# Kernel tuning notes

Measured on AMD Instinct MI355X. Metric: run time of the kernel, lower is better.

Reference implementation:

```python
import jax, jax.numpy as jnp
import numpy as np
import math

B, LS, G, KNN, DIM, PE, H, DH = 2, 2048, 32, 16, 256, 32, 8, 32
INNER = H * DH
FF = 4 * DIM
EPS = 1e-5


def _ln(x, g, b):
    m = jnp.mean(x, -1, keepdims=True)
    v = jnp.var(x, -1, keepdims=True)
    return (x - m) / jnp.sqrt(v + EPS) * g + b


def _ff(x, w1, b1, w2, b2):
    return jax.nn.gelu(x @ w1 + b1) @ w2 + b2


def setup_inputs():
    key = jax.random.key(0)
    ks = jax.random.split(key, 20)
    def w(i, shape):
        return jax.random.normal(ks[i], shape, jnp.float32) * 0.02
    return {
        'latents': jax.random.normal(ks[0], (B, LS + G, DIM), jnp.float32),
        'topk_indices': jax.random.randint(ks[1], (B, LS, KNN), 0, LS),
        'rpe': jax.random.normal(ks[2], (B, LS, KNN, PE), jnp.float32),
        'self_rpe': jax.random.normal(ks[3], (B, LS, 1, PE), jnp.float32),
        'distances': jax.random.uniform(ks[4], (B, LS, KNN), jnp.float32) * 10.0,
        'num_spatial': LS,
        'sa_wq': w(5, (DIM, INNER)), 'sa_wk': w(6, (DIM + PE, INNER)),
        'sa_wv': w(7, (DIM + PE, INNER)), 'sa_wo': w(8, (INNER, DIM)),
        'sa_bo': jnp.zeros((DIM,)),
        'sa_log_sigma': jnp.full((H,), math.log(3.0), jnp.float32),
        'sa_gbias': jnp.asarray(0.0, jnp.float32),
        'ln1_g': jnp.ones((DIM,)), 'ln1_b': jnp.zeros((DIM,)),
        'ln2_g': jnp.ones((DIM,)), 'ln2_b': jnp.zeros((DIM,)),
        'sff_w1': w(9, (DIM, FF)), 'sff_b1': jnp.zeros((FF,)),
        'sff_w2': w(10, (FF, DIM)), 'sff_b2': jnp.zeros((DIM,)),
        'ga_wq': w(11, (DIM, INNER)), 'ga_wk': w(12, (DIM, INNER)),
        'ga_wv': w(13, (DIM, INNER)), 'ga_wo': w(14, (INNER, DIM)),
        'ga_bo': jnp.zeros((DIM,)),
        'ga_gbias': jnp.asarray(0.0, jnp.float32),
        'ln3_g': jnp.ones((DIM,)), 'ln3_b': jnp.zeros((DIM,)),
        'ln4_g': jnp.ones((DIM,)), 'ln4_b': jnp.zeros((DIM,)),
        'gff_w1': w(15, (DIM, FF)), 'gff_b1': jnp.zeros((FF,)),
        'gff_w2': w(16, (FF, DIM)), 'gff_b2': jnp.zeros((DIM,)),
    }


def _forward(latents, topk_indices, rpe, self_rpe, distances, num_spatial, p):
    L = num_spatial
    spatial = latents[:, :L]
    glob = latents[:, L:]
    b, _, d = spatial.shape
    g = glob.shape[1]
    scale = DH ** -0.5
    # ---- spatial local attention: context = [self, kNN neighbors, all globals] ----
    x = _ln(spatial, p['ln1_g'], p['ln1_b'])
    neighbors = jax.vmap(lambda s, idx: s[idx])(x, topk_indices)  # [B,L,k,D] gather
    glob_exp = jnp.broadcast_to(glob[:, None], (b, L, g, d))
    ctx = jnp.concatenate([x[:, :, None, :], neighbors, glob_exp], axis=2)  # [B,L,1+k+G,D]
    rpe_cat = jnp.concatenate([self_rpe, rpe, jnp.zeros((b, L, g, PE), x.dtype)], axis=2)
    ctx = jnp.concatenate([ctx, rpe_cat], axis=-1)  # [B,L,C,D+PE]
    q = (x @ p['sa_wq']).reshape(b, L, H, DH)
    kk = (ctx @ p['sa_wk']).reshape(b, L, -1, H, DH)
    vv = (ctx @ p['sa_wv']).reshape(b, L, -1, H, DH)
    attn = jnp.einsum('blhd,blchd->bhlc', q, kk) * scale
    sigma_sq = jnp.exp(2.0 * p['sa_log_sigma'])  # [H]
    dist_sp = jnp.concatenate([jnp.zeros((b, L, 1), x.dtype), distances], axis=2)  # [B,L,1+k]
    gauss = -(dist_sp ** 2)[:, None] / (2.0 * sigma_sq[None, :, None, None])  # [B,H,L,1+k]
    bias = jnp.concatenate([gauss, jnp.broadcast_to(p['sa_gbias'], (b, H, L, g))], axis=-1)
    attn = jax.nn.softmax(attn + bias, axis=-1)
    out = jnp.einsum('bhlc,blchd->blhd', attn, vv).reshape(b, L, INNER)
    spatial = spatial + out @ p['sa_wo'] + p['sa_bo']
    spatial = spatial + _ff(_ln(spatial, p['ln2_g'], p['ln2_b']), p['sff_w1'], p['sff_b1'], p['sff_w2'], p['sff_b2'])
    # ---- global full attention: Q=global, K/V=[updated spatial; normed global] ----
    gq_in = _ln(glob, p['ln3_g'], p['ln3_b'])
    kv = jnp.concatenate([spatial, gq_in], axis=1)  # [B,L+G,D]
    qg = (gq_in @ p['ga_wq']).reshape(b, g, H, DH)
    kg = (kv @ p['ga_wk']).reshape(b, L + g, H, DH)
    vg = (kv @ p['ga_wv']).reshape(b, L + g, H, DH)
    a2 = jnp.einsum('bghd,bchd->bhgc', qg, kg) * scale + p['ga_gbias']
    a2 = jax.nn.softmax(a2, axis=-1)
    og = jnp.einsum('bhgc,bchd->bghd', a2, vg).reshape(b, g, INNER)
    glob = glob + og @ p['ga_wo'] + p['ga_bo']
    glob = glob + _ff(_ln(glob, p['ln4_g'], p['ln4_b']), p['gff_w1'], p['gff_b1'], p['gff_w2'], p['gff_b2'])
    return jnp.concatenate([spatial, glob], axis=1)


def reference(latents, topk_indices, rpe, self_rpe, distances, num_spatial,
              sa_wq, sa_wk, sa_wv, sa_wo, sa_bo, sa_log_sigma, sa_gbias,
              ln1_g, ln1_b, ln2_g, ln2_b, sff_w1, sff_b1, sff_w2, sff_b2,
              ga_wq, ga_wk, ga_wv, ga_wo, ga_bo, ga_gbias,
              ln3_g, ln3_b, ln4_g, ln4_b, gff_w1, gff_b1, gff_w2, gff_b2):
    p = dict(sa_wq=sa_wq, sa_wk=sa_wk, sa_wv=sa_wv, sa_wo=sa_wo, sa_bo=sa_bo,
             sa_log_sigma=sa_log_sigma, sa_gbias=sa_gbias,
             ln1_g=ln1_g, ln1_b=ln1_b, ln2_g=ln2_g, ln2_b=ln2_b,
             sff_w1=sff_w1, sff_b1=sff_b1, sff_w2=sff_w2, sff_b2=sff_b2,
             ga_wq=ga_wq, ga_wk=ga_wk, ga_wv=ga_wv, ga_wo=ga_wo, ga_bo=ga_bo,
             ga_gbias=ga_gbias, ln3_g=ln3_g, ln3_b=ln3_b, ln4_g=ln4_g, ln4_b=ln4_b,
             gff_w1=gff_w1, gff_b1=gff_b1, gff_w2=gff_w2, gff_b2=gff_b2)
    return _forward(latents, topk_indices, rpe, self_rpe, distances, num_spatial, p)
```

## Files before the change

kernel.cpp:

```cpp
#include <hip/hip_runtime.h>
#include <math.h>

#define LS 2048
#define NG 32
#define ROWS_B 2080
#define DIM 256
#define PE 32
#define NH 8
#define DH 32
#define NCTX 49
#define SCALE 0.17677669529663687f

typedef __attribute__((ext_vector_type(8))) short short8;
typedef __attribute__((ext_vector_type(4))) float f32x4;
typedef __attribute__((ext_vector_type(4))) unsigned short us4;

__device__ __forceinline__ unsigned short f2bf(float x)
{
    unsigned int u = __float_as_uint(x);
    unsigned int r = (u + 0x7fffu + ((u >> 16) & 1u)) >> 16;
    return (unsigned short)r;
}
__device__ __forceinline__ float bf2f(unsigned short v)
{
    return __uint_as_float((unsigned int)v << 16);
}
__device__ __forceinline__ float4 bf2f4(us4 v)
{
    return (float4){ bf2f(v.x), bf2f(v.y), bf2f(v.z), bf2f(v.w) };
}
__device__ __forceinline__ float dot4(float4 a, float4 b)
{
    return a.x * b.x + a.y * b.y + a.z * b.z + a.w * b.w;
}
__device__ __forceinline__ float gelu_f(float x)
{
    float x3 = x * x * x;
    return 0.5f * x * (1.0f + tanhf(0.7978845608028654f * (x + 0.044715f * x3)));
}

struct WEnt { const float* src; unsigned short* dst; int K; int N; int t0; };
struct WTab { WEnt e[9]; };

__global__ __launch_bounds__(256) void wprep_k(
    WTab tab,
    const float* __restrict__ sa_wq, const float* __restrict__ sa_wk,
    const float* __restrict__ sa_wv, const float* __restrict__ sa_wo,
    unsigned short* __restrict__ wt_qkvw, unsigned short* __restrict__ wt_wo2,
    const float* __restrict__ latents,
    const float* __restrict__ g1, const float* __restrict__ b1,
    const float* __restrict__ g3, const float* __restrict__ b3,
    float* __restrict__ X, float* __restrict__ GQ)
{
    __shared__ unsigned short tile[64][72];
    __shared__ float red[8];
    int blk = blockIdx.x, t = threadIdx.x;
    if (blk < 512) {
        const float* wkpe = sa_wk + 256 * 256;
        const float* wvpe = sa_wv + 256 * 256;
        if (blk < 256) {
            int j = blk, h = j >> 5, p = j & 31;
            const float* wq = sa_wq + (size_t)t * 256 + h * 32;
            const float* wk = wkpe + (size_t)p * 256 + h * 32;
            float acc = 0.0f;
            #pragma unroll
            for (int dd = 0; dd < 32; ++dd) acc += wq[dd] * wk[dd];
            wt_qkvw[(size_t)(768 + j) * 256 + t] = f2bf(acc);
        } else {
            int n = blk - 256;
            #pragma unroll
            for (int kk = 0; kk < 2; ++kk) {
                int k = t + kk * 256;
                float v;
                if (k < 256) v = sa_wo[(size_t)k * 256 + n];
                else {
                    int j = k - 256, h = j >> 5, p = j & 31;
                    float a = 0.0f;
                    #pragma unroll
                    for (int dd = 0; dd < 32; ++dd)
                        a += wvpe[(size_t)p * 256 + h * 32 + dd] * sa_wo[(size_t)(h * 32 + dd) * 256 + n];
                    v = a;
                }
                wt_wo2[(size_t)n * 512 + k] = f2bf(v);
            }
        }
    } else if (blk < 736) {
        int local0 = blk - 512;
        int i = 0;
        #pragma unroll
        for (int j = 1; j < 9; ++j) if (local0 >= tab.e[j].t0) i = j;
        const float* W = tab.e[i].src;
        unsigned short* Wt = tab.e[i].dst;
        int K = tab.e[i].K, N = tab.e[i].N;
        int local = local0 - tab.e[i].t0;
        int nb = N >> 6;
        int n0 = (local % nb) * 64, k0 = (local / nb) * 64;
        #pragma unroll
        for (int r = 0; r < 4; ++r) {
            int k = r * 16 + (t >> 4);
            int n = (t & 15) * 4;
            float4 wv = *(const float4*)(W + (size_t)(k0 + k) * N + n0 + n);
            tile[k][n + 0] = f2bf(wv.x);
            tile[k][n + 1] = f2bf(wv.y);
            tile[k][n + 2] = f2bf(wv.z);
            tile[k][n + 3] = f2bf(wv.w);
        }
        __syncthreads();
        #pragma unroll
        for (int r = 0; r < 4; ++r) {
            int n = r * 16 + (t >> 4);
            int k = (t & 15) * 4;
            us4 o;
            o.x = tile[k + 0][n];
            o.y = tile[k + 1][n];
            o.z = tile[k + 2][n];
            o.w = tile[k + 3][n];
            *(us4*)(Wt + (size_t)(n0 + n) * K + k0 + k) = o;
        }
    } else {
        int blk2 = blk - 736;
        const float* gam; const float* bet; size_t ip; float* op;
        if (blk2 < 4096) {
            int b = blk2 >> 11;
            ip = ((size_t)b * ROWS_B + (blk2 & 2047)) * DIM + t;
            op = X + (size_t)blk2 * DIM + t;
            gam = g1; bet = b1;
        } else {
            int r2 = blk2 - 4096;
            int b = r2 >> 5;
            ip = ((size_t)b * ROWS_B + LS + (r2 & 31)) * DIM + t;
            op = GQ + (size_t)r2 * DIM + t;
            gam = g3; bet = b3;
        }
        float v = latents[ip];
        float a = v, b2 = v * v;
        #pragma unroll
        for (int m = 32; m >= 1; m >>= 1) { a += __shfl_xor(a, m); b2 += __shfl_xor(b2, m); }
        if ((t & 63) == 0) { red[t >> 6] = a; red[4 + (t >> 6)] = b2; }
        __syncthreads();
        float mean = (red[0] + red[1] + red[2] + red[3]) * (1.0f / 256.0f);
        float var  = (red[4] + red[5] + red[6] + red[7]) * (1.0f / 256.0f) - mean * mean;
        *op = (v - mean) * rsqrtf(var + 1e-5f) * gam[t] + bet[t];
    }
}

__global__ __launch_bounds__(256) void ln_rows_k(
    const float* __restrict__ in, const float* __restrict__ gam,
    const float* __restrict__ bet, float* __restrict__ out)
{
    __shared__ float red[8];
    int r = blockIdx.x, t = threadIdx.x;
    int b = r >> 11;
    size_t ip = ((size_t)b * ROWS_B + (r & 2047)) * DIM + t;
    float v = in[ip];
    float a = v, b2 = v * v;
    #pragma unroll
    for (int m = 32; m >= 1; m >>= 1) { a += __shfl_xor(a, m); b2 += __shfl_xor(b2, m); }
    if ((t & 63) == 0) { red[t >> 6] = a; red[4 + (t >> 6)] = b2; }
    __syncthreads();
    float mean = (red[0] + red[1] + red[2] + red[3]) * (1.0f / 256.0f);
    float var  = (red[4] + red[5] + red[6] + red[7]) * (1.0f / 256.0f) - mean * mean;
    out[(size_t)r * DIM + t] = (v - mean) * rsqrtf(var + 1e-5f) * gam[t] + bet[t];
}

__global__ __launch_bounds__(256) void wgs_k(
    const unsigned short* __restrict__ wtq, const unsigned short* __restrict__ kvglb,
    unsigned short* __restrict__ wgs)
{
    int n = blockIdx.x, k = threadIdx.x;
    int h = n & 7, cg = n >> 3;
    float acc = 0.0f;
    #pragma unroll
    for (int dd = 0; dd < 32; ++dd)
        acc += bf2f(wtq[(size_t)(h * 32 + dd) * 256 + k]) * bf2f(kvglb[(size_t)cg * 512 + h * 32 + dd]);
    wgs[(size_t)n * 256 + k] = f2bf(acc);
}

template<int BIAS, int DOGELU, int RES, int ABF16, int CBF16>
__global__ __launch_bounds__(256) void mgemm_k(
    const void* __restrict__ Av, const unsigned short* __restrict__ Bt,
    const float* __restrict__ bias, const float* __restrict__ Res,
    void* __restrict__ Cv, int M, int N, int K, int bstr,
    int arpb, int absr, int aoff, int crpb, int cbsr, int coff)
{
    __shared__ unsigned short Asl[64][64];
    __shared__ unsigned short Bsl[64][64];
    int t = threadIdx.x;
    int col0 = blockIdx.x * 64, row0 = blockIdx.y * 64;
    int lane = t & 63, w = t >> 6;
    int wr = w >> 1, wc = w & 1;
    int lrow = lane & 15, lk = lane >> 4;

    int srow = t >> 4;
    int scol = (t & 15) << 2;
    int sslot = (t & 15) >> 1;
    int shalf = (t & 15) & 1;

    f32x4 acc[2][2];
    #pragma unroll
    for (int m = 0; m < 2; ++m)
        #pragma unroll
        for (int n = 0; n < 2; ++n)
            acc[m][n] = (f32x4){0.f, 0.f, 0.f, 0.f};

    for (int kk = 0; kk < K; kk += 64) {
        #pragma unroll
        for (int r = 0; r < 4; ++r) {
            int row = r * 16 + srow;
            int ar = row0 + row;
            size_t ab = ((size_t)(ar / arpb) * absr + aoff + (ar % arpb)) * (size_t)K + kk + scol;
            us4 ap;
            if (ABF16) {
                ap = *(const us4*)((const unsigned short*)Av + ab);
            } else {
                float4 av = *(const float4*)((const float*)Av + ab);
                ap.x = f2bf(av.x); ap.y = f2bf(av.y); ap.z = f2bf(av.z); ap.w = f2bf(av.w);
            }
            *(us4*)&Asl[row][((sslot ^ (row & 7)) << 3) + (shalf << 2)] = ap;
            us4 bv = *(const us4*)(Bt + (size_t)(col0 + row) * bstr + kk + scol);
            *(us4*)&Bsl[row][((sslot ^ (row & 7)) << 3) + (shalf << 2)] = bv;
        }
        __syncthreads();
        #pragma unroll
        for (int k2 = 0; k2 < 2; ++k2) {
            short8 af[2], bfr[2];
            #pragma unroll
            for (int m = 0; m < 2; ++m) {
                int rowA = wr * 32 + m * 16 + lrow;
                af[m] = *(short8*)&Asl[rowA][((k2 * 4 + lk) ^ (rowA & 7)) << 3];
                int rowB = wc * 32 + m * 16 + lrow;
                bfr[m] = *(short8*)&Bsl[rowB][((k2 * 4 + lk) ^ (rowB & 7)) << 3];
            }
            #pragma unroll
            for (int m = 0; m < 2; ++m)
                #pragma unroll
                for (int n = 0; n < 2; ++n)
                    acc[m][n] = __builtin_amdgcn_mfma_f32_16x16x32_bf16(af[m], bfr[n], acc[m][n], 0, 0, 0);
        }
        __syncthreads();
    }
    #pragma unroll
    for (int m = 0; m < 2; ++m) {
        #pragma unroll
        for (int n = 0; n < 2; ++n) {
            int col = col0 + wc * 32 + n * 16 + lrow;
            #pragma unroll
            for (int j = 0; j < 4; ++j) {
                int r = row0 + wr * 32 + m * 16 + lk * 4 + j;
                size_t cp = ((size_t)(r / crpb) * cbsr + coff + (r % crpb)) * (size_t)N + col;
                float o = acc[m][n][j];
                if (BIAS)   o += bias[col];
                if (DOGELU) o = gelu_f(o);
                if (RES)    o += Res[cp];
                if (CBF16) ((unsigned short*)Cv)[cp] = f2bf(o);
                else       ((float*)Cv)[cp] = o;
            }
        }
    }
}

__global__ __launch_bounds__(256) void attn_sp_k(
    const unsigned short* __restrict__ QKV, const unsigned short* __restrict__ KVGLb,
    const unsigned short* __restrict__ GSb, const int* __restrict__ idx,
    const float* __restrict__ rpe, const float* __restrict__ srpe,
    const float* __restrict__ dist, const float* __restrict__ lsig,
    const float* __restrict__ gbias, unsigned short* __restrict__ ORb)
{
    __shared__ float s_rpe[17 * 32];
    __shared__ float s_sc[NCTX * 8];
    __shared__ float s_red[32 * 64];
    __shared__ float s_d[16];
    __shared__ int   s_row[17];
    int t = threadIdx.x;
    int r = blockIdx.x;
    int b = r >> 11;
    int w = t >> 6, lane = t & 63;
    int h = lane >> 3, dg = lane & 7;

    if (t < 32) s_rpe[t] = srpe[(size_t)r * 32 + t];
    for (int i = t; i < 512; i += 256) s_rpe[32 + i] = rpe[(size_t)r * 512 + i];
    if (t < 16) {
        s_row[t + 1] = (b << 11) + idx[r * 16 + t];
        s_d[t] = dist[(size_t)r * 16 + t];
    }
    if (t == 16) s_row[0] = r;

    size_t qb = (size_t)r * 1024 + lane * 4;
    float4 q4  = bf2f4(*(const us4*)(QKV + qb));
    float4 qw4 = bf2f4(*(const us4*)(QKV + qb + 768));
    float inv2s = 1.0f / (2.0f * __expf(2.0f * lsig[h]));
    float gb = gbias[0];
    __syncthreads();

    us4 kreg[5];
    #pragma unroll
    for (int i = 0; i < 5; ++i) {
        int c = w + 4 * i;
        if (c < 17) kreg[i] = *(const us4*)(QKV + (size_t)s_row[c] * 1024 + 256 + lane * 4);
    }
    float sc_loc[5];
    #pragma unroll
    for (int i = 0; i < 5; ++i) {
        int c = w + 4 * i;
        if (c < 17) {
            float4 k4 = bf2f4(kreg[i]);
            float4 rv4 = *(const float4*)&s_rpe[c * 32 + dg * 4];
            float part = dot4(q4, k4) + dot4(rv4, qw4);
            part += __shfl_xor(part, 1);
            part += __shfl_xor(part, 2);
            part += __shfl_xor(part, 4);
            float bia = (c == 0) ? 0.0f : -s_d[c - 1] * s_d[c - 1] * inv2s;
            float sval = part * SCALE + bia;
            if (dg == 0) s_sc[c * 8 + h] = sval;
            sc_loc[i] = sval;
        }
    }
    float sc_glob[8];
    #pragma unroll
    for (int i = 0; i < 8; ++i) {
        int gi = w + 4 * i;
        float sval = bf2f(GSb[(size_t)r * 512 + (((size_t)b * 32 + gi) << 3) + h]) * SCALE + gb;
        if (dg == 0) s_sc[(17 + gi) * 8 + h] = sval;
        sc_glob[i] = sval;
    }
    __syncthreads();

    float vals[7];
    float lm = -3.0e38f;
    #pragma unroll
    for (int i = 0; i < 7; ++i) {
        int cc = dg + 8 * i;
        if (cc < NCTX) { float v = s_sc[cc * 8 + h]; vals[i] = v; lm = fmaxf(lm, v); }
    }
    lm = fmaxf(lm, __shfl_xor(lm, 1));
    lm = fmaxf(lm, __shfl_xor(lm, 2));
    lm = fmaxf(lm, __shfl_xor(lm, 4));
    float ls = 0.0f;
    #pragma unroll
    for (int i = 0; i < 7; ++i) {
        int cc = dg + 8 * i;
        if (cc < NCTX) ls += __expf(vals[i] - lm);
    }
    ls += __shfl_xor(ls, 1);
    ls += __shfl_xor(ls, 2);
    ls += __shfl_xor(ls, 4);
    float inv = 1.0f / ls;

    us4 vreg[5];
    #pragma unroll
    for (int i = 0; i < 5; ++i) {
        int c = w + 4 * i;
        if (c < 17) vreg[i] = *(const us4*)(QKV + (size_t)s_row[c] * 1024 + 512 + lane * 4);
    }
    float4 acc4 = (float4){0, 0, 0, 0}, racc4 = (float4){0, 0, 0, 0};
    #pragma unroll
    for (int i = 0; i < 5; ++i) {
        int c = w + 4 * i;
        if (c < 17) {
            float p = __expf(sc_loc[i] - lm);
            float4 v4 = bf2f4(vreg[i]);
            float4 rv4 = *(const float4*)&s_rpe[c * 32 + dg * 4];
            racc4.x += p * rv4.x; racc4.y += p * rv4.y;
            racc4.z += p * rv4.z; racc4.w += p * rv4.w;
            acc4.x += p * v4.x; acc4.y += p * v4.y;
            acc4.z += p * v4.z; acc4.w += p * v4.w;
        }
    }
    #pragma unroll
    for (int i = 0; i < 8; ++i) {
        int gi = w + 4 * i;
        float p = __expf(sc_glob[i] - lm);
        float4 v4 = bf2f4(*(const us4*)(KVGLb + ((size_t)(b * NG + gi)) * 512 + 256 + lane * 4));
        acc4.x += p * v4.x; acc4.y += p * v4.y;
        acc4.z += p * v4.z; acc4.w += p * v4.w;
    }

    s_red[(w * 8 + 0) * 64 + lane] = acc4.x;
    s_red[(w * 8 + 1) * 64 + lane] = acc4.y;
    s_red[(w * 8 + 2) * 64 + lane] = acc4.z;
    s_red[(w * 8 + 3) * 64 + lane] = acc4.w;
    s_red[(w * 8 + 4) * 64 + lane] = racc4.x;
    s_red[(w * 8 + 5) * 64 + lane] = racc4.y;
    s_red[(w * 8 + 6) * 64 + lane] = racc4.z;
    s_red[(w * 8 + 7) * 64 + lane] = racc4.w;
    __syncthreads();
    {
        int j = w;
        float a = 0.0f, rr = 0.0f;
        #pragma unroll
        for (int ww = 0; ww < 4; ++ww) {
            a  += s_red[(ww * 8 + j) * 64 + lane];
            rr += s_red[(ww * 8 + 4 + j) * 64 + lane];
        }
        int e = h * 32 + dg * 4 + j;
        ORb[(size_t)r * 512 + e]       = f2bf(a * inv);
        ORb[(size_t)r * 512 + 256 + e] = f2bf(rr * inv);
    }
}

__global__ __launch_bounds__(256) void ga_scores_k(
    const unsigned short* __restrict__ GKVQ, const unsigned short* __restrict__ KVG,
    float* __restrict__ A2)
{
    int t = threadIdx.x;
    int bh = blockIdx.x;
    int b = bh >> 3, h = bh & 7;
    int w = t >> 6, lane = t & 63;
    int ct = blockIdx.y * 4 + w;
    if (ct >= 130) return;
    int lr = lane & 15, lq = lane >> 4;

    short8 aq0 = *(const short8*)(GKVQ + ((size_t)(b * 32 + lr)) * 768 + 512 + h * 32 + lq * 8);
    short8 aq1 = *(const short8*)(GKVQ + ((size_t)(b * 32 + 16 + lr)) * 768 + 512 + h * 32 + lq * 8);
    int c = ct * 16 + lr;
    const unsigned short* kr = (c < LS)
        ? KVG + ((size_t)(b * LS + c)) * 512 + h * 32 + lq * 8
        : GKVQ + ((size_t)(b * NG + (c - LS))) * 768 + h * 32 + lq * 8;
    short8 bk = *(const short8*)kr;

    f32x4 acc0 = (f32x4){0, 0, 0, 0}, acc1 = (f32x4){0, 0, 0, 0};
    acc0 = __builtin_amdgcn_mfma_f32_16x16x32_bf16(aq0, bk, acc0, 0, 0, 0);
    acc1 = __builtin_amdgcn_mfma_f32_16x16x32_bf16(aq1, bk, acc1, 0, 0, 0);

    float* arow = A2 + ((size_t)(b * NH + h) * NG) * ROWS_B + ct * 16 + lr;
    #pragma unroll
    for (int j = 0; j < 4; ++j) {
        arow[(size_t)(lq * 4 + j) * ROWS_B]        = acc0[j] * SCALE;
        arow[(size_t)(16 + lq * 4 + j) * ROWS_B]   = acc1[j] * SCALE;
    }
}

__global__ __launch_bounds__(256) void ga_softmax_k(float* __restrict__ A2)
{
    __shared__ float red[8];
    int t = threadIdx.x;
    float* row = A2 + (size_t)blockIdx.x * ROWS_B;
    float lm = -1e30f;
    for (int i = t; i < ROWS_B; i += 256) lm = fmaxf(lm, row[i]);
    #pragma unroll
    for (int m = 32; m >= 1; m >>= 1) lm = fmaxf(lm, __shfl_xor(lm, m));
    if ((t & 63) == 0) red[t >> 6] = lm;
    __syncthreads();
    float M = fmaxf(fmaxf(red[0], red[1]), fmaxf(red[2], red[3]));
    float ls = 0.0f;
    for (int i = t; i < ROWS_B; i += 256) {
        float e = __expf(row[i] - M);
        row[i] = e;
        ls += e;
    }
    #pragma unroll
    for (int m = 32; m >= 1; m >>= 1) ls += __shfl_xor(ls, m);
    if ((t & 63) == 0) red[4 + (t >> 6)] = ls;
    __syncthreads();
    float inv = 1.0f / (red[4] + red[5] + red[6] + red[7]);
    for (int i = t; i < ROWS_B; i += 256) row[i] *= inv;
}

__global__ __launch_bounds__(256) void ga_wv_k(
    const float* __restrict__ A2, const unsigned short* __restrict__ GKVQ,
    const unsigned short* __restrict__ KVG, float* __restrict__ OGP)
{
    __shared__ float s_acc[8][256];
    int t = threadIdx.x;
    int bg = blockIdx.x;
    int s = blockIdx.y;
    int b = bg >> 5, g = bg & 31;
    int tt = t & 31, sub = t >> 5;
    int h = tt >> 2;
    const float* w = A2 + ((size_t)(b * NH + h) * NG + g) * ROWS_B;
    int c0 = s * 65, cend = c0 + 65;
    float acc[8] = {};
    for (int c = c0 + sub; c < cend; c += 8) {
        float p = w[c];
        const unsigned short* vr = (c < LS)
            ? KVG + ((size_t)(b * LS + c)) * 512 + 256 + tt * 8
            : GKVQ + ((size_t)(b * NG + (c - LS))) * 768 + 256 + tt * 8;
        us4 v0 = *(const us4*)vr;
        us4 v1 = *(const us4*)(vr + 4);
        acc[0] += p * bf2f(v0.x); acc[1] += p * bf2f(v0.y);
        acc[2] += p * bf2f(v0.z); acc[3] += p * bf2f(v0.w);
        acc[4] += p * bf2f(v1.x); acc[5] += p * bf2f(v1.y);
        acc[6] += p * bf2f(v1.z); acc[7] += p * bf2f(v1.w);
    }
    #pragma unroll
    for (int j = 0; j < 8; ++j) s_acc[sub][tt * 8 + j] = acc[j];
    __syncthreads();
    float o = 0.0f;
    #pragma unroll
    for (int ss = 0; ss < 8; ++ss) o += s_acc[ss][t];
    OGP[((size_t)bg * 32 + s) * 256 + t] = o;
}

__global__ __launch_bounds__(1024) void glob_tail_k(
    const float* __restrict__ OGP, const float* __restrict__ latents,
    const float* __restrict__ ga_wo, const float* __restrict__ ga_bo,
    const float* __restrict__ ln4g, const float* __restrict__ ln4b,
    const float* __restrict__ w1, const float* __restrict__ b1,
    const float* __restrict__ w2, const float* __restrict__ b2,
    float* __restrict__ GTP)
{
    __shared__ float s_part[4][256];
    __shared__ float s_og[256];
    __shared__ float s_y[256];
    __shared__ float s_h1[256];
    __shared__ float red[16];
    int bg = blockIdx.x, q = blockIdx.y, t = threadIdx.x;
    int tt = t & 255, grp = t >> 8;

    float og = 0.0f;
    #pragma unroll
    for (int s = 0; s < 8; ++s)
        og += OGP[((size_t)bg * 32 + grp * 8 + s) * 256 + tt];
    s_part[grp][tt] = og;
    __syncthreads();
    if (grp == 0) s_og[tt] = s_part[0][tt] + s_part[1][tt] + s_part[2][tt] + s_part[3][tt];
    __syncthreads();

    float x = 0.0f;
    {
        int k0 = grp * 64;
        #pragma unroll 16
        for (int k = k0; k < k0 + 64; ++k) x += s_og[k] * ga_wo[(size_t)k * 256 + tt];
    }
    s_part[grp][tt] = x;
    __syncthreads();
    int b = bg >> 5;
    size_t row = (size_t)b * ROWS_B + LS + (bg & 31);
    float res = latents[row * 256 + tt]
              + s_part[0][tt] + s_part[1][tt] + s_part[2][tt] + s_part[3][tt] + ga_bo[tt];

    float a = res, b2s = res * res;
    #pragma unroll
    for (int m = 32; m >= 1; m >>= 1) { a += __shfl_xor(a, m); b2s += __shfl_xor(b2s, m); }
    if ((t & 63) == 0 && t < 256) { red[t >> 6] = a; red[8 + (t >> 6)] = b2s; }
    __syncthreads();
    float mean = (red[0] + red[1] + red[2] + red[3]) * (1.0f / 256.0f);
    float var  = (red[8] + red[9] + red[10] + red[11]) * (1.0f / 256.0f) - mean * mean;
    float y = (res - mean) * rsqrtf(var + 1e-5f) * ln4g[tt] + ln4b[tt];
    if (grp == 0) s_y[tt] = y;
    __syncthreads();

    float h1p = 0.0f;
    {
        int k0 = grp * 64;
        #pragma unroll 16
        for (int k = k0; k < k0 + 64; ++k) h1p += s_y[k] * w1[(size_t)k * 1024 + q * 256 + tt];
    }
    s_part[grp][tt] = h1p;
    __syncthreads();
    if (grp == 0)
        s_h1[tt] = gelu_f(b1[q * 256 + tt]
                 + s_part[0][tt] + s_part[1][tt] + s_part[2][tt] + s_part[3][tt]);
    __syncthreads();

    float o = 0.0f;
    {
        int j0 = grp * 64;
        #pragma unroll 16
        for (int j = j0; j < j0 + 64; ++j) o += s_h1[j] * w2[(size_t)(q * 256 + j) * 256 + tt];
    }
    s_part[grp][tt] = o;
    __syncthreads();
    if (grp == 0) {
        float v = s_part[0][tt] + s_part[1][tt] + s_part[2][tt] + s_part[3][tt];
        if (q == 0) v += res + b2[tt];
        GTP[((size_t)bg * 4 + q) * 256 + tt] = v;
    }
}

__global__ __launch_bounds__(256) void glob_fin_k(
    const float* __restrict__ GTP, float* __restrict__ out)
{
    int bg = blockIdx.x, t = threadIdx.x;
    int b = bg >> 5;
    size_t row = (size_t)b * ROWS_B + LS + (bg & 31);
    float v = GTP[((size_t)bg * 4 + 0) * 256 + t] + GTP[((size_t)bg * 4 + 1) * 256 + t]
            + GTP[((size_t)bg * 4 + 2) * 256 + t] + GTP[((size_t)bg * 4 + 3) * 256 + t];
    out[row * 256 + t] = v;
}

extern "C" void kernel_launch(void* const* d_in, const int* in_sizes, int n_in,
                              void* d_out, int out_size, void* d_ws, size_t ws_size,
                              hipStream_t stream)
{
    const float* latents = (const float*)d_in[0];
    const int*   idx     = (const int*)d_in[1];
    const float* rpe     = (const float*)d_in[2];
    const float* srpe    = (const float*)d_in[3];
    const float* dist    = (const float*)d_in[4];
    const float* sa_wq   = (const float*)d_in[6];
    const float* sa_wk   = (const float*)d_in[7];
    const float* sa_wv   = (const float*)d_in[8];
    const float* sa_wo   = (const float*)d_in[9];
    const float* sa_bo   = (const float*)d_in[10];
    const float* lsig    = (const float*)d_in[11];
    const float* gbias   = (const float*)d_in[12];
    const float* ln1g    = (const float*)d_in[13];
    const float* ln1b    = (const float*)d_in[14];
    const float* ln2g    = (const float*)d_in[15];
    const float* ln2b    = (const float*)d_in[16];
    const float* sff_w1  = (const float*)d_in[17];
    const float* sff_b1  = (const float*)d_in[18];
    const float* sff_w2  = (const float*)d_in[19];
    const float* sff_b2  = (const float*)d_in[20];
    const float* ga_wq   = (const float*)d_in[21];
    const float* ga_wk   = (const float*)d_in[22];
    const float* ga_wv   = (const float*)d_in[23];
    const float* ga_wo   = (const float*)d_in[24];
    const float* ga_bo   = (const float*)d_in[25];
    const float* ln3g    = (const float*)d_in[27];
    const float* ln3b    = (const float*)d_in[28];
    const float* ln4g    = (const float*)d_in[29];
    const float* ln4b    = (const float*)d_in[30];
    const float* gff_w1  = (const float*)d_in[31];
    const float* gff_b1  = (const float*)d_in[32];
    const float* gff_w2  = (const float*)d_in[33];
    const float* gff_b2  = (const float*)d_in[34];
    float* out = (float*)d_out;

    const size_t SZ = (size_t)4096 * 256;
    float* ws = (float*)d_ws;
    float* X = ws;
    unsigned short* QKVb = (unsigned short*)(ws + SZ);
    unsigned short* H1b  = QKVb;
    unsigned short* KVGb = QKVb;
    unsigned short* ORb  = (unsigned short*)(ws + 3 * SZ);
    unsigned short* GSb  = (unsigned short*)(ws + 4 * SZ);
    float* A2  = ws + 3 * SZ;
    float* OGP = A2 + (size_t)2 * NH * NG * ROWS_B;
    float* GTP = OGP + (size_t)64 * 32 * 256;
    unsigned short* wt = (unsigned short*)(ws + 5 * SZ);
    unsigned short* wt_qkvw = wt;
    unsigned short* wt_ff1  = wt + 262144;
    unsigned short* wt_ff2  = wt + 524288;
    unsigned short* wt_gakv = wt + 786432;
    unsigned short* wt_wo2  = wt + 983040;
    unsigned short* wgs_w   = wt + 1114112;
    float* smalls = ws + 5 * SZ + 622592;
    unsigned short* KVGLb = (unsigned short*)smalls;
    float* GQ = smalls + 16384;
    unsigned short* GKVQb = (unsigned short*)(GQ + 16384);

    dim3 blk(256);

    WTab tab;
    tab.e[0] = { sa_wq,  wt_qkvw,           256,  256,   0 };
    tab.e[1] = { sa_wk,  wt_qkvw + 65536,   256,  256,  16 };
    tab.e[2] = { sa_wv,  wt_qkvw + 131072,  256,  256,  32 };
    tab.e[3] = { sff_w1, wt_ff1,            256, 1024,  48 };
    tab.e[4] = { sff_w2, wt_ff2,           1024,  256, 112 };
    tab.e[5] = { ga_wk,  wt_gakv,           256,  256, 176 };
    tab.e[6] = { ga_wv,  wt_gakv + 65536,   256,  256, 192 };
    tab.e[7] = { ga_wq,  wt_gakv + 131072,  256,  256, 208 };
    tab.e[8] = { sa_wq,  wt_qkvw,           256,  256, 1 << 30 };

    wprep_k<<<dim3(4896), blk, 0, stream>>>(tab, sa_wq, sa_wk, sa_wv, sa_wo,
                                            wt_qkvw, wt_wo2, latents,
                                            ln1g, ln1b, ln3g, ln3b, X, GQ);

    mgemm_k<0,0,0,0,1><<<dim3(8,1), blk, 0, stream>>>(latents, wt_qkvw + 65536, nullptr, nullptr, KVGLb,
        64,512,256,256, 32,ROWS_B,LS, 64,64,0);
    wgs_k<<<dim3(512), blk, 0, stream>>>(wt_qkvw, KVGLb, wgs_w);

    mgemm_k<0,0,0,0,1><<<dim3(16,64), blk, 0, stream>>>(X, wt_qkvw, nullptr, nullptr, QKVb,
        4096,1024,256,256, 4096,4096,0, 4096,4096,0);
    mgemm_k<0,0,0,0,1><<<dim3(8,64), blk, 0, stream>>>(X, wgs_w, nullptr, nullptr, GSb,
        4096,512,256,256, 4096,4096,0, 4096,4096,0);

    attn_sp_k<<<dim3(4096), blk, 0, stream>>>(QKVb, KVGLb, GSb, idx, rpe, srpe, dist,
                                              lsig, gbias, ORb);

    mgemm_k<1,0,1,1,0><<<dim3(4,64), blk, 0, stream>>>(ORb, wt_wo2, sa_bo, latents, out,
        4096,256,512,512, 4096,4096,0, LS,ROWS_B,0);

    ln_rows_k<<<dim3(4096), blk, 0, stream>>>(out, ln2g, ln2b, X);
    mgemm_k<1,1,0,0,1><<<dim3(16,64), blk, 0, stream>>>(X, wt_ff1, sff_b1, nullptr, H1b,
        4096,1024,256,256, 4096,4096,0, 4096,4096,0);
    mgemm_k<1,0,1,1,0><<<dim3(4,64), blk, 0, stream>>>(H1b, wt_ff2, sff_b2, out, out,
        4096,256,1024,1024, 4096,4096,0, LS,ROWS_B,0);

    mgemm_k<0,0,0,0,1><<<dim3(8,64), blk, 0, stream>>>(out, wt_gakv, nullptr, nullptr, KVGb,
        4096,512,256,256, LS,ROWS_B,0, 4096,4096,0);
    mgemm_k<0,0,0,0,1><<<dim3(12,1), blk, 0, stream>>>(GQ, wt_gakv, nullptr, nullptr, GKVQb,
        64,768,256,256, 64,64,0, 64,64,0);

    ga_scores_k<<<dim3(16, 33), blk, 0, stream>>>(GKVQb, KVGb, A2);
    ga_softmax_k<<<dim3(512), blk, 0, stream>>>(A2);
    ga_wv_k<<<dim3(64, 32), blk, 0, stream>>>(A2, GKVQb, KVGb, OGP);

    glob_tail_k<<<dim3(64, 4), dim3(1024), 0, stream>>>(OGP, latents, ga_wo, ga_bo, ln4g, ln4b,
                                                        gff_w1, gff_b1, gff_w2, gff_b2, GTP);
    glob_fin_k<<<dim3(64), blk, 0, stream>>>(GTP, out);
}
```

Measured before the change: 169.9 us.

## Fuse QKV and global-score GEMMs and switch large GEMMs to 128-row tiles

The global-score projection weights are placed right after the QKV weights, so a single GEMM writes a 1536-wide row holding Q, K, V, QW and the global scores. The attention kernel now reads the scores from that combined buffer at a new stride. A new 128x64-tile MFMA GEMM replaces the 64x64 version for the large projections, reusing B tiles over more rows and halving the block count. Each block carries more accumulators, which may lower occupancy, and the grids shrink to 128–768 blocks.

```diff
diff --git a/kernel.cpp b/kernel.cpp
--- a/kernel.cpp
+++ b/kernel.cpp
@@ -10,6 +10,7 @@
 #define DH 32
 #define NCTX 49
 #define SCALE 0.17677669529663687f
+#define QSTR 1536
 
 typedef __attribute__((ext_vector_type(8))) short short8;
 typedef __attribute__((ext_vector_type(4))) float f32x4;
@@ -259,12 +260,102 @@
     }
 }
 
+template<int BIAS, int DOGELU, int RES, int ABF16, int CBF16>
+__global__ __launch_bounds__(256) void mgemm128_k(
+    const void* __restrict__ Av, const unsigned short* __restrict__ Bt,
+    const float* __restrict__ bias, const float* __restrict__ Res,
+    void* __restrict__ Cv, int M, int N, int K, int bstr,
+    int arpb, int absr, int aoff, int crpb, int cbsr, int coff)
+{
+    __shared__ unsigned short Asl[128][64];
+    __shared__ unsigned short Bsl[64][64];
+    int t = threadIdx.x;
+    int col0 = blockIdx.x * 64, row0 = blockIdx.y * 128;
+    int lane = t & 63, w = t >> 6;
+    int wr = w >> 1, wc = w & 1;
+    int lrow = lane & 15, lk = lane >> 4;
+
+    int srow = t >> 4;
+    int scol = (t & 15) << 2;
+    int sslot = (t & 15) >> 1;
+    int shalf = (t & 15) & 1;
+
+    f32x4 acc[4][2];
+    #pragma unroll
+    for (int m = 0; m < 4; ++m)
+        #pragma unroll
+        for (int n = 0; n < 2; ++n)
+            acc[m][n] = (f32x4){0.f, 0.f, 0.f, 0.f};
+
+    for (int kk = 0; kk < K; kk += 64) {
+        #pragma unroll
+        for (int r = 0; r < 8; ++r) {
+            int row = r * 16 + srow;
+            int ar = row0 + row;
+            size_t ab = ((size_t)(ar / arpb) * absr + aoff + (ar % arpb)) * (size_t)K + kk + scol;
+            us4 ap;
+            if (ABF16) {
+                ap = *(const us4*)((const unsigned short*)Av + ab);
+            } else {
+                float4 av = *(const float4*)((const float*)Av + ab);
+                ap.x = f2bf(av.x); ap.y = f2bf(av.y); ap.z = f2bf(av.z); ap.w = f2bf(av.w);
+            }
+            *(us4*)&Asl[row][((sslot ^ (row & 7)) << 3) + (shalf << 2)] = ap;
+        }
+        #pragma unroll
+        for (int r = 0; r < 4; ++r) {
+            int row = r * 16 + srow;
+            us4 bv = *(const us4*)(Bt + (size_t)(col0 + row) * bstr + kk + scol);
+            *(us4*)&Bsl[row][((sslot ^ (row & 7)) << 3) + (shalf << 2)] = bv;
+        }
+        __syncthreads();
+        #pragma unroll
+        for (int k2 = 0; k2 < 2; ++k2) {
+            short8 af[4], bfr[2];
+            #pragma unroll
+            for (int m = 0; m < 4; ++m) {
+                int rowA = wr * 64 + m * 16 + lrow;
+                af[m] = *(short8*)&Asl[rowA][((k2 * 4 + lk) ^ (rowA & 7)) << 3];
+            }
+            #pragma unroll
+            for (int n = 0; n < 2; ++n) {
+                int rowB = wc * 32 + n * 16 + lrow;
+                bfr[n] = *(short8*)&Bsl[rowB][((k2 * 4 + lk) ^ (rowB & 7)) << 3];
+            }
+            #pragma unroll
+            for (int m = 0; m < 4; ++m)
+                #pragma unroll
+                for (int n = 0; n < 2; ++n)
+                    acc[m][n] = __builtin_amdgcn_mfma_f32_16x16x32_bf16(af[m], bfr[n], acc[m][n], 0, 0, 0);
+        }
+        __syncthreads();
+    }
+    #pragma unroll
+    for (int m = 0; m < 4; ++m) {
+        #pragma unroll
+        for (int n = 0; n < 2; ++n) {
+            int col = col0 + wc * 32 + n * 16 + lrow;
+            #pragma unroll
+            for (int j = 0; j < 4; ++j) {
+                int r = row0 + wr * 64 + m * 16 + lk * 4 + j;
+                size_t cp = ((size_t)(r / crpb) * cbsr + coff + (r % crpb)) * (size_t)N + col;
+                float o = acc[m][n][j];
+                if (BIAS)   o += bias[col];
+                if (DOGELU) o = gelu_f(o);
+                if (RES)    o += Res[cp];
+                if (CBF16) ((unsigned short*)Cv)[cp] = f2bf(o);
+                else       ((float*)Cv)[cp] = o;
+            }
+        }
+    }
+}
+
 __global__ __launch_bounds__(256) void attn_sp_k(
     const unsigned short* __restrict__ QKV, const unsigned short* __restrict__ KVGLb,
-    const unsigned short* __restrict__ GSb, const int* __restrict__ idx,
-    const float* __restrict__ rpe, const float* __restrict__ srpe,
-    const float* __restrict__ dist, const float* __restrict__ lsig,
-    const float* __restrict__ gbias, unsigned short* __restrict__ ORb)
+    const int* __restrict__ idx, const float* __restrict__ rpe,
+    const float* __restrict__ srpe, const float* __restrict__ dist,
+    const float* __restrict__ lsig, const float* __restrict__ gbias,
+    unsigned short* __restrict__ ORb)
 {
     __shared__ float s_rpe[17 * 32];
     __shared__ float s_sc[NCTX * 8];
@@ -285,7 +376,7 @@
     }
     if (t == 16) s_row[0] = r;
 
-    size_t qb = (size_t)r * 1024 + lane * 4;
+    size_t qb = (size_t)r * QSTR + lane * 4;
     float4 q4  = bf2f4(*(const us4*)(QKV + qb));
     float4 qw4 = bf2f4(*(const us4*)(QKV + qb + 768));
     float inv2s = 1.0f / (2.0f * __expf(2.0f * lsig[h]));
@@ -296,7 +387,7 @@
     #pragma unroll
     for (int i = 0; i < 5; ++i) {
         int c = w + 4 * i;
-        if (c < 17) kreg[i] = *(const us4*)(QKV + (size_t)s_row[c] * 1024 + 256 + lane * 4);
+        if (c < 17) kreg[i] = *(const us4*)(QKV + (size_t)s_row[c] * QSTR + 256 + lane * 4);
     }
     float sc_loc[5];
     #pragma unroll
@@ -319,7 +410,7 @@
     #pragma unroll
     for (int i = 0; i < 8; ++i) {
         int gi = w + 4 * i;
-        float sval = bf2f(GSb[(size_t)r * 512 + (((size_t)b * 32 + gi) << 3) + h]) * SCALE + gb;
+        float sval = bf2f(QKV[(size_t)r * QSTR + 1024 + (((size_t)b * 32 + gi) << 3) + h]) * SCALE + gb;
         if (dg == 0) s_sc[(17 + gi) * 8 + h] = sval;
         sc_glob[i] = sval;
     }
@@ -350,7 +441,7 @@
     #pragma unroll
     for (int i = 0; i < 5; ++i) {
         int c = w + 4 * i;
-        if (c < 17) vreg[i] = *(const us4*)(QKV + (size_t)s_row[c] * 1024 + 512 + lane * 4);
+        if (c < 17) vreg[i] = *(const us4*)(QKV + (size_t)s_row[c] * QSTR + 512 + lane * 4);
     }
     float4 acc4 = (float4){0, 0, 0, 0}, racc4 = (float4){0, 0, 0, 0};
     #pragma unroll
@@ -621,22 +712,21 @@
     const size_t SZ = (size_t)4096 * 256;
     float* ws = (float*)d_ws;
     float* X = ws;
-    unsigned short* QKVb = (unsigned short*)(ws + SZ);
-    unsigned short* H1b  = QKVb;
-    unsigned short* KVGb = QKVb;
-    unsigned short* ORb  = (unsigned short*)(ws + 3 * SZ);
-    unsigned short* GSb  = (unsigned short*)(ws + 4 * SZ);
-    float* A2  = ws + 3 * SZ;
+    unsigned short* QKV2b = (unsigned short*)(ws + SZ);
+    unsigned short* H1b  = QKV2b;
+    unsigned short* KVGb = QKV2b;
+    unsigned short* ORb  = (unsigned short*)(ws + 4 * SZ);
+    float* A2  = ws + 5 * SZ;
     float* OGP = A2 + (size_t)2 * NH * NG * ROWS_B;
     float* GTP = OGP + (size_t)64 * 32 * 256;
-    unsigned short* wt = (unsigned short*)(ws + 5 * SZ);
+    unsigned short* wt = (unsigned short*)(ws + 7 * SZ);
     unsigned short* wt_qkvw = wt;
-    unsigned short* wt_ff1  = wt + 262144;
-    unsigned short* wt_ff2  = wt + 524288;
-    unsigned short* wt_gakv = wt + 786432;
-    unsigned short* wt_wo2  = wt + 983040;
-    unsigned short* wgs_w   = wt + 1114112;
-    float* smalls = ws + 5 * SZ + 622592;
+    unsigned short* wgs_w   = wt + 262144;
+    unsigned short* wt_ff1  = wt + 393216;
+    unsigned short* wt_ff2  = wt + 655360;
+    unsigned short* wt_gakv = wt + 917504;
+    unsigned short* wt_wo2  = wt + 1114112;
+    float* smalls = ws + 8 * SZ;
     unsigned short* KVGLb = (unsigned short*)smalls;
     float* GQ = smalls + 16384;
     unsigned short* GKVQb = (unsigned short*)(GQ + 16384);
@@ -662,24 +752,22 @@
         64,512,256,256, 32,ROWS_B,LS, 64,64,0);
     wgs_k<<<dim3(512), blk, 0, stream>>>(wt_qkvw, KVGLb, wgs_w);
 
-    mgemm_k<0,0,0,0,1><<<dim3(16,64), blk, 0, stream>>>(X, wt_qkvw, nullptr, nullptr, QKVb,
+    mgemm128_k<0,0,0,0,1><<<dim3(24,32), blk, 0, stream>>>(X, wt_qkvw, nullptr, nullptr, QKV2b,
+        4096,QSTR,256,256, 4096,4096,0, 4096,4096,0);
+
+    attn_sp_k<<<dim3(4096), blk, 0, stream>>>(QKV2b, KVGLb, idx, rpe, srpe, dist,
+                                              lsig, gbias, ORb);
+
+    mgemm128_k<1,0,1,1,0><<<dim3(4,32), blk, 0, stream>>>(ORb, wt_wo2, sa_bo, latents, out,
+        4096,256,512,512, 4096,4096,0, LS,ROWS_B,0);
+
+    ln_rows_k<<<dim3(4096), blk, 0, stream>>>(out, ln2g, ln2b, X);
+    mgemm128_k<1,1,0,0,1><<<dim3(16,32), blk, 0, stream>>>(X, wt_ff1, sff_b1, nullptr, H1b,
         4096,1024,256,256, 4096,4096,0, 4096,4096,0);
-    mgemm_k<0,0,0,0,1><<<dim3(8,64), blk, 0, stream>>>(X, wgs_w, nullptr, nullptr, GSb,
-        4096,512,256,256, 4096,4096,0, 4096,4096,0);
-
-    attn_sp_k<<<dim3(4096), blk, 0, stream>>>(QKVb, KVGLb, GSb, idx, rpe, srpe, dist,
-                                              lsig, gbias, ORb);
-
-    mgemm_k<1,0,1,1,0><<<dim3(4,64), blk, 0, stream>>>(ORb, wt_wo2, sa_bo, latents, out,
-        4096,256,512,512, 4096,4096,0, LS,ROWS_B,0);
-
-    ln_rows_k<<<dim3(4096), blk, 0, stream>>>(out, ln2g, ln2b, X);
-    mgemm_k<1,1,0,0,1><<<dim3(16,64), blk, 0, stream>>>(X, wt_ff1, sff_b1, nullptr, H1b,
-        4096,1024,256,256, 4096,4096,0, 4096,4096,0);
-    mgemm_k<1,0,1,1,0><<<dim3(4,64), blk, 0, stream>>>(H1b, wt_ff2, sff_b2, out, out,
+    mgemm128_k<1,0,1,1,0><<<dim3(4,32), blk, 0, stream>>>(H1b, wt_ff2, sff_b2, out, out,
         4096,256,1024,1024, 4096,4096,0, LS,ROWS_B,0);
 
-    mgemm_k<0,0,0,0,1><<<dim3(8,64), blk, 0, stream>>>(out, wt_gakv, nullptr, nullptr, KVGb,
+    mgemm128_k<0,0,0,0,1><<<dim3(8,32), blk, 0, stream>>>(out, wt_gakv, nullptr, nullptr, KVGb,
         4096,512,256,256, LS,ROWS_B,0, 4096,4096,0);
     mgemm_k<0,0,0,0,1><<<dim3(12,1), blk, 0, stream>>>(GQ, wt_gakv, nullptr, nullptr, GKVQb,
         64,768,256,256, 64,64,0, 64,64,0);
```

After: 182.4 us. 7.3% more time.
